# Performance work log

Hardware: AMD Instinct MI355X
Metric: run time of the kernel (lower is better)

## Reference

```python
import jax, jax.numpy as jnp
import numpy as np

ALPHA = 0.1
EPS = 1e-7

def proj(x):
    # Re-project onto hyperboloid: time coord t = sqrt(1 + |s|^2)
    s = x[:, 1:]
    t = jnp.sqrt(1.0 + jnp.sum(s * s, axis=-1, keepdims=True))
    return jnp.concatenate([t, s], axis=-1)

def linner(x, y):
    # Lorentzian inner product <x,y>_L = -x0*y0 + <xs, ys>
    return -x[..., 0] * y[..., 0] + jnp.sum(x[..., 1:] * y[..., 1:], axis=-1)

def safe_acosh(z):
    return jnp.arccosh(jnp.maximum(z, 1.0 + EPS))

def setup_inputs() -> dict:
    key = jax.random.key(0)
    k1, k2 = jax.random.split(key)
    B, n, A = 1_000_000, 64, 16
    s = jax.random.normal(k1, (B, n), dtype=jnp.float32) * 0.5
    t = jnp.sqrt(1.0 + jnp.sum(s * s, axis=-1, keepdims=True))
    hyp_emb = jnp.concatenate([t, s], axis=-1)  # [B, n+1] on hyperboloid
    a_s = jax.random.normal(k2, (A, n), dtype=jnp.float32) * 0.01
    a_t = jnp.sqrt(1.0 + jnp.sum(a_s * a_s, axis=-1, keepdims=True))
    anchors = jnp.concatenate([a_t, a_s], axis=-1)  # [A, n+1]
    return {"hyp_emb": hyp_emb, "anchors": anchors}

def reference(hyp_emb, anchors):
    anchors_p = proj(anchors)  # [A, d]
    # Lorentzian pairwise inner products [B, A]
    inner = (-hyp_emb[:, :1] * anchors_p[None, :, 0]
             + jnp.einsum('bd,ad->ba', hyp_emb[:, 1:], anchors_p[:, 1:]))
    dists = safe_acosh(-inner)
    nearest_idx = jnp.argmin(dists, axis=1)        # [B]
    na = anchors_p[nearest_idx]                    # [B, d] gather
    # log_map_x(y): d(x,y) * (y + <x,y> x) / ||y + <x,y> x||_L
    xy = linner(hyp_emb, na)                       # [B]
    d = safe_acosh(-xy)
    u = na + xy[:, None] * hyp_emb
    unorm = jnp.sqrt(jnp.maximum(linner(u, u), EPS))
    v = (ALPHA * d / unorm)[:, None] * u           # alpha * direction
    # exp_map_x(v): cosh(|v|) x + sinh(|v|) v / |v|
    vn = jnp.sqrt(jnp.maximum(linner(v, v), EPS * EPS))
    sinhc = jnp.where(vn > EPS, jnp.sinh(vn) / vn, 1.0)
    out = jnp.cosh(vn)[:, None] * hyp_emb + sinhc[:, None] * v
    return out
```

## Files before the change

### kernel.cpp

```cpp
#include <hip/hip_runtime.h>
#include <math.h>
#include <stdint.h>

#define ALPHA 0.1f
#define EPS 1e-7f

constexpr int D = 65;
constexpr int A = 16;
constexpr int RPW = 64;
constexpr int TILE_FLOATS = RPW * D;
constexpr int NBLOCKS = 1024;

__device__ __forceinline__ void async_cp16(const float* g, float* l) {
    __builtin_amdgcn_global_load_lds(
        (const __attribute__((address_space(1))) uint32_t*)(uintptr_t)g,
        (__attribute__((address_space(3))) uint32_t*)(uint32_t)(uintptr_t)l,
        16, 0, 0);
}
__device__ __forceinline__ void async_cp4(const float* g, float* l) {
    __builtin_amdgcn_global_load_lds(
        (const __attribute__((address_space(1))) uint32_t*)(uintptr_t)g,
        (__attribute__((address_space(3))) uint32_t*)(uint32_t)(uintptr_t)l,
        4, 0, 0);
}

__global__ void prep_anchors(const float* __restrict__ anchors,
                             float* __restrict__ ws) {
    __shared__ float s_a[A * D];
    int tid = threadIdx.x;
    for (int i = tid; i < A * D; i += blockDim.x) s_a[i] = anchors[i];
    __syncthreads();
    if (tid < A) {
        float s = 0.f;
        for (int j = 1; j < D; ++j) {
            float v = s_a[tid * D + j];
            s = fmaf(v, v, s);
        }
        s_a[tid * D] = sqrtf(1.f + s);
    }
    __syncthreads();
    for (int i = tid; i < A * D; i += blockDim.x) {
        int a = i / D, j = i % D;
        ws[j * A + a] = s_a[i];
        ws[A * D + i] = s_a[i];
    }
}

__device__ __forceinline__ void row_math(const float xr[D],
                                         const float* __restrict__ aT,
                                         const float* __restrict__ anch,
                                         float* __restrict__ orow) {
    float acc[A];
#pragma unroll
    for (int a = 0; a < A; ++a) acc[a] = -xr[0] * aT[a];
#pragma unroll
    for (int j = 1; j < D; ++j) {
        const float xj = xr[j];
#pragma unroll
        for (int a = 0; a < A; ++a)
            acc[a] = fmaf(xj, aT[j * A + a], acc[a]);
    }

    const float onePlusEps = 1.0f + EPS;
    float bestZ = fmaxf(-acc[0], onePlusEps);
    float xy = acc[0];
    int bidx = 0;
#pragma unroll
    for (int a = 1; a < A; ++a) {
        float z = fmaxf(-acc[a], onePlusEps);
        if (z < bestZ) { bestZ = z; bidx = a; xy = acc[a]; }
    }
    const float d = acoshf(bestZ);

    const float* na = anch + bidx * D;
    float uu;
    {
        float u0 = fmaf(xy, xr[0], na[0]);
        uu = -u0 * u0;
    }
#pragma unroll
    for (int j = 1; j < D; ++j) {
        float uj = fmaf(xy, xr[j], na[j]);
        uu = fmaf(uj, uj, uu);
    }
    const float unorm = sqrtf(fmaxf(uu, EPS));
    const float c = ALPHA * d / unorm;
    const float vv = c * c * uu;
    const float vn = sqrtf(fmaxf(vv, EPS * EPS));
    const float sinhc = (vn > EPS) ? (sinhf(vn) / vn) : 1.0f;
    const float ch = coshf(vn);
    const float sc = sinhc * c;
    const float k1 = fmaf(sc, xy, ch);
#pragma unroll
    for (int j = 0; j < D; ++j)
        orow[j] = fmaf(k1, xr[j], sc * na[j]);
}

__global__ __launch_bounds__(64, 1) void
homeo_kernel(const float* __restrict__ x,
             const float* __restrict__ aT,
             const float* __restrict__ aRM,
             float* __restrict__ out, int B) {
    __shared__ float buf[2][TILE_FLOATS];
    __shared__ float anch[A * D];

    const int lane = threadIdx.x;
    const long stride = gridDim.x;
    const int nTiles = (B + RPW - 1) / RPW;

    for (int i = lane; i < A * D; i += 64) anch[i] = aRM[i];

    {
        const long t0 = blockIdx.x;
        if (t0 < nTiles && (t0 + 1) * (long)RPW <= (long)B) {
            const float* g = x + t0 * (long)TILE_FLOATS;
#pragma unroll
            for (int c = 0; c < 16; ++c)
                async_cp16(g + c * 256 + lane * 4, buf[0] + c * 256);
            async_cp4(g + 16 * 256 + lane, buf[0] + 16 * 256);
        }
    }
    __syncthreads();

    int p = 0;
    for (long t = blockIdx.x; t < nTiles; t += stride, p ^= 1) {
        const long rowStart = t * RPW;
        const int nRows = (int)min((long)RPW, (long)B - rowStart);

        {
            const long tn = t + stride;
            if (tn < nTiles && (tn + 1) * (long)RPW <= (long)B) {
                const float* g = x + tn * (long)TILE_FLOATS;
                float* l = buf[p ^ 1];
#pragma unroll
                for (int c = 0; c < 16; ++c)
                    async_cp16(g + c * 256 + lane * 4, l + c * 256);
                async_cp4(g + 16 * 256 + lane, l + 16 * 256);
            }
        }
        asm volatile("s_waitcnt vmcnt(17)" ::: "memory");

        float* lbase = buf[p];
        if (nRows == RPW) {
            float xr[D];
#pragma unroll
            for (int j = 0; j < D; ++j) xr[j] = lbase[lane * D + j];

            row_math(xr, aT, anch, lbase + lane * D);

            asm volatile("s_waitcnt lgkmcnt(0)" ::: "memory");

            float4* o4 = (float4*)(out + rowStart * (long)D);
            const float4* l4 = (const float4*)lbase;
#pragma unroll
            for (int c2 = 0; c2 < 16; ++c2)
                o4[c2 * 64 + lane] = l4[c2 * 64 + lane];
            out[rowStart * (long)D + 16 * 256 + lane] = lbase[16 * 256 + lane];
        } else if (lane < nRows) {
            const float* xg = x + (rowStart + lane) * (long)D;
            float xr[D];
            for (int j = 0; j < D; ++j) xr[j] = xg[j];
            row_math(xr, aT, anch, out + (rowStart + lane) * (long)D);
        }
    }
}

extern "C" void kernel_launch(void* const* d_in, const int* in_sizes, int n_in,
                              void* d_out, int out_size, void* d_ws, size_t ws_size,
                              hipStream_t stream) {
    const float* hyp = (const float*)d_in[0];
    const float* anchors = (const float*)d_in[1];
    float* out = (float*)d_out;
    float* ws = (float*)d_ws;

    const int B = in_sizes[0] / D;
    const int nTiles = (B + RPW - 1) / RPW;
    const int grid = nTiles < NBLOCKS ? nTiles : NBLOCKS;

    prep_anchors<<<1, 256, 0, stream>>>(anchors, ws);
    homeo_kernel<<<grid, 64, 0, stream>>>(hyp, ws, ws + A * D, out, B);
}
```

Baseline: 445.6 us.

## Replace async LDS double buffer with register-staged prefetch and single LDS tile

Drops the global_load_lds async copies into a double-buffered LDS tile. The next tile is now prefetched into registers (16 float4 plus a tail) while the current tile is computed, then written into a single LDS buffer afterwards. Halving the LDS footprint lets the grid grow from 1024 to 1792 blocks for more resident waves. The cost is about 65 extra VGPRs per thread for the staging registers, on top of a kernel that already holds a 65-float row and 16 accumulators, which risks spilling or lower occupancy.

```diff
diff --git a/kernel.cpp b/kernel.cpp
--- a/kernel.cpp
+++ b/kernel.cpp
@@ -9,20 +9,7 @@
 constexpr int A = 16;
 constexpr int RPW = 64;
 constexpr int TILE_FLOATS = RPW * D;
-constexpr int NBLOCKS = 1024;
-
-__device__ __forceinline__ void async_cp16(const float* g, float* l) {
-    __builtin_amdgcn_global_load_lds(
-        (const __attribute__((address_space(1))) uint32_t*)(uintptr_t)g,
-        (__attribute__((address_space(3))) uint32_t*)(uint32_t)(uintptr_t)l,
-        16, 0, 0);
-}
-__device__ __forceinline__ void async_cp4(const float* g, float* l) {
-    __builtin_amdgcn_global_load_lds(
-        (const __attribute__((address_space(1))) uint32_t*)(uintptr_t)g,
-        (__attribute__((address_space(3))) uint32_t*)(uint32_t)(uintptr_t)l,
-        4, 0, 0);
-}
+constexpr int NBLOCKS = 1792;
 
 __global__ void prep_anchors(const float* __restrict__ anchors,
                              float* __restrict__ ws) {
@@ -101,7 +88,7 @@
              const float* __restrict__ aT,
              const float* __restrict__ aRM,
              float* __restrict__ out, int B) {
-    __shared__ float buf[2][TILE_FLOATS];
+    __shared__ float buf[TILE_FLOATS];
     __shared__ float anch[A * D];
 
     const int lane = threadIdx.x;
@@ -110,57 +97,65 @@
 
     for (int i = lane; i < A * D; i += 64) anch[i] = aRM[i];
 
+    float4 sv[16];
+    float stail = 0.f;
+
     {
         const long t0 = blockIdx.x;
         if (t0 < nTiles && (t0 + 1) * (long)RPW <= (long)B) {
             const float* g = x + t0 * (long)TILE_FLOATS;
 #pragma unroll
             for (int c = 0; c < 16; ++c)
-                async_cp16(g + c * 256 + lane * 4, buf[0] + c * 256);
-            async_cp4(g + 16 * 256 + lane, buf[0] + 16 * 256);
+                sv[c] = *reinterpret_cast<const float4*>(g + (c * 64 + lane) * 4);
+            stail = g[16 * 256 + lane];
+#pragma unroll
+            for (int c = 0; c < 16; ++c)
+                *reinterpret_cast<float4*>(buf + (c * 64 + lane) * 4) = sv[c];
+            buf[16 * 256 + lane] = stail;
         }
     }
-    __syncthreads();
 
-    int p = 0;
-    for (long t = blockIdx.x; t < nTiles; t += stride, p ^= 1) {
+    for (long t = blockIdx.x; t < nTiles; t += stride) {
         const long rowStart = t * RPW;
         const int nRows = (int)min((long)RPW, (long)B - rowStart);
 
-        {
-            const long tn = t + stride;
-            if (tn < nTiles && (tn + 1) * (long)RPW <= (long)B) {
-                const float* g = x + tn * (long)TILE_FLOATS;
-                float* l = buf[p ^ 1];
+        const long tn = t + stride;
+        const bool pre = (tn < nTiles) && ((tn + 1) * (long)RPW <= (long)B);
+        if (pre) {
+            const float* g = x + tn * (long)TILE_FLOATS;
 #pragma unroll
-                for (int c = 0; c < 16; ++c)
-                    async_cp16(g + c * 256 + lane * 4, l + c * 256);
-                async_cp4(g + 16 * 256 + lane, l + 16 * 256);
-            }
+            for (int c = 0; c < 16; ++c)
+                sv[c] = *reinterpret_cast<const float4*>(g + (c * 64 + lane) * 4);
+            stail = g[16 * 256 + lane];
         }
-        asm volatile("s_waitcnt vmcnt(17)" ::: "memory");
 
-        float* lbase = buf[p];
         if (nRows == RPW) {
             float xr[D];
 #pragma unroll
-            for (int j = 0; j < D; ++j) xr[j] = lbase[lane * D + j];
+            for (int j = 0; j < D; ++j) xr[j] = buf[lane * D + j];
 
-            row_math(xr, aT, anch, lbase + lane * D);
+            row_math(xr, aT, anch, buf + lane * D);
 
             asm volatile("s_waitcnt lgkmcnt(0)" ::: "memory");
 
             float4* o4 = (float4*)(out + rowStart * (long)D);
-            const float4* l4 = (const float4*)lbase;
+            const float4* l4 = (const float4*)buf;
 #pragma unroll
             for (int c2 = 0; c2 < 16; ++c2)
                 o4[c2 * 64 + lane] = l4[c2 * 64 + lane];
-            out[rowStart * (long)D + 16 * 256 + lane] = lbase[16 * 256 + lane];
+            out[rowStart * (long)D + 16 * 256 + lane] = buf[16 * 256 + lane];
         } else if (lane < nRows) {
             const float* xg = x + (rowStart + lane) * (long)D;
             float xr[D];
             for (int j = 0; j < D; ++j) xr[j] = xg[j];
             row_math(xr, aT, anch, out + (rowStart + lane) * (long)D);
+        }
+
+        if (pre) {
+#pragma unroll
+            for (int c = 0; c < 16; ++c)
+                *reinterpret_cast<float4*>(buf + (c * 64 + lane) * 4) = sv[c];
+            buf[16 * 256 + lane] = stail;
         }
     }
 }
```

After: 486.0 us. 1.09x slower.

## Replace persistent double-buffered grid with one block per tile

Applied to the files above, without the earlier changes.

Drops the persistent 1024-block grid and its in-block double-buffered async prefetch. It launches one 64-thread block per 64-row tile, each with a single LDS buffer. Latency is meant to be hidden by having many more resident wavefronts per CU rather than by software pipelining, and the smaller LDS footprint per block allows more of them. In exchange, every block reloads the anchors and pays launch overhead, and the explicit vmcnt wait before reading the async-loaded tile is gone, so correctness relies on the compiler inserting it.

```diff
diff --git a/kernel.cpp b/kernel.cpp
--- a/kernel.cpp
+++ b/kernel.cpp
@@ -9,7 +9,6 @@
 constexpr int A = 16;
 constexpr int RPW = 64;
 constexpr int TILE_FLOATS = RPW * D;
-constexpr int NBLOCKS = 1024;
 
 __device__ __forceinline__ void async_cp16(const float* g, float* l) {
     __builtin_amdgcn_global_load_lds(
@@ -101,67 +100,45 @@
              const float* __restrict__ aT,
              const float* __restrict__ aRM,
              float* __restrict__ out, int B) {
-    __shared__ float buf[2][TILE_FLOATS];
+    __shared__ float buf[TILE_FLOATS];
     __shared__ float anch[A * D];
 
     const int lane = threadIdx.x;
-    const long stride = gridDim.x;
-    const int nTiles = (B + RPW - 1) / RPW;
+    const long t = blockIdx.x;
+    const long rowStart = t * RPW;
+    const int nRows = (int)min((long)RPW, (long)B - rowStart);
+    const bool full = (nRows == RPW);
+
+    if (full) {
+        const float* g = x + rowStart * (long)D;
+#pragma unroll
+        for (int c = 0; c < 16; ++c)
+            async_cp16(g + c * 256 + lane * 4, buf + c * 256);
+        async_cp4(g + 16 * 256 + lane, buf + 16 * 256);
+    }
 
     for (int i = lane; i < A * D; i += 64) anch[i] = aRM[i];
 
-    {
-        const long t0 = blockIdx.x;
-        if (t0 < nTiles && (t0 + 1) * (long)RPW <= (long)B) {
-            const float* g = x + t0 * (long)TILE_FLOATS;
+    if (full) {
+        float xr[D];
 #pragma unroll
-            for (int c = 0; c < 16; ++c)
-                async_cp16(g + c * 256 + lane * 4, buf[0] + c * 256);
-            async_cp4(g + 16 * 256 + lane, buf[0] + 16 * 256);
-        }
-    }
-    __syncthreads();
+        for (int j = 0; j < D; ++j) xr[j] = buf[lane * D + j];
 
-    int p = 0;
-    for (long t = blockIdx.x; t < nTiles; t += stride, p ^= 1) {
-        const long rowStart = t * RPW;
-        const int nRows = (int)min((long)RPW, (long)B - rowStart);
+        row_math(xr, aT, anch, buf + lane * D);
 
-        {
-            const long tn = t + stride;
-            if (tn < nTiles && (tn + 1) * (long)RPW <= (long)B) {
-                const float* g = x + tn * (long)TILE_FLOATS;
-                float* l = buf[p ^ 1];
+        asm volatile("s_waitcnt lgkmcnt(0)" ::: "memory");
+
+        float4* o4 = (float4*)(out + rowStart * (long)D);
+        const float4* l4 = (const float4*)buf;
 #pragma unroll
-                for (int c = 0; c < 16; ++c)
-                    async_cp16(g + c * 256 + lane * 4, l + c * 256);
-                async_cp4(g + 16 * 256 + lane, l + 16 * 256);
-            }
-        }
-        asm volatile("s_waitcnt vmcnt(17)" ::: "memory");
-
-        float* lbase = buf[p];
-        if (nRows == RPW) {
-            float xr[D];
-#pragma unroll
-            for (int j = 0; j < D; ++j) xr[j] = lbase[lane * D + j];
-
-            row_math(xr, aT, anch, lbase + lane * D);
-
-            asm volatile("s_waitcnt lgkmcnt(0)" ::: "memory");
-
-            float4* o4 = (float4*)(out + rowStart * (long)D);
-            const float4* l4 = (const float4*)lbase;
-#pragma unroll
-            for (int c2 = 0; c2 < 16; ++c2)
-                o4[c2 * 64 + lane] = l4[c2 * 64 + lane];
-            out[rowStart * (long)D + 16 * 256 + lane] = lbase[16 * 256 + lane];
-        } else if (lane < nRows) {
-            const float* xg = x + (rowStart + lane) * (long)D;
-            float xr[D];
-            for (int j = 0; j < D; ++j) xr[j] = xg[j];
-            row_math(xr, aT, anch, out + (rowStart + lane) * (long)D);
-        }
+        for (int c2 = 0; c2 < 16; ++c2)
+            o4[c2 * 64 + lane] = l4[c2 * 64 + lane];
+        out[rowStart * (long)D + 16 * 256 + lane] = buf[16 * 256 + lane];
+    } else if (lane < nRows) {
+        const float* xg = x + (rowStart + lane) * (long)D;
+        float xr[D];
+        for (int j = 0; j < D; ++j) xr[j] = xg[j];
+        row_math(xr, aT, anch, out + (rowStart + lane) * (long)D);
     }
 }
 
@@ -175,8 +152,7 @@
 
     const int B = in_sizes[0] / D;
     const int nTiles = (B + RPW - 1) / RPW;
-    const int grid = nTiles < NBLOCKS ? nTiles : NBLOCKS;
 
     prep_anchors<<<1, 256, 0, stream>>>(anchors, ws);
-    homeo_kernel<<<grid, 64, 0, stream>>>(hyp, ws, ws + A * D, out, B);
+    homeo_kernel<<<nTiles, 64, 0, stream>>>(hyp, ws, ws + A * D, out, B);
 }
```

New measurement: 440.5 us. Within noise of the previous version (-1.1%).
